# Performance work log

Measured on AMD Instinct MI355X. Metric: run time of the kernel, lower is better.

The kernel has to match this reference:

```python
import jax, jax.numpy as jnp
import numpy as np

B, T, N, F = 4096, 64, 8, 4
H = 64           # GRU hidden
EID = 16         # id embedding dim
CM = 32          # comm message dim
D = H + EID + CM # 112, attention dim
INV_SQRT_D = 1.0 / np.sqrt(112.0)


def setup_inputs() -> dict:
    key = jax.random.key(0)
    ks = jax.random.split(key, 24)
    def rn(k, shape, s=0.05):
        return jax.random.normal(k, shape, jnp.float32) * s
    return {
        "seq": jax.random.normal(ks[0], (B, T, N, F), jnp.float32),
        # GRU (torch layout: W_ih [3H,F], W_hh [3H,H], gates ordered r,z,n)
        "W_ih": rn(ks[1], (3 * H, F)), "W_hh": rn(ks[2], (3 * H, H)),
        "b_ih": rn(ks[3], (3 * H,)), "b_hh": rn(ks[4], (3 * H,)),
        "embed": rn(ks[5], (8, EID)),
        "Wm": rn(ks[6], (CM, H + EID)), "bm": rn(ks[7], (CM,)),
        "Wq": rn(ks[8], (D, D)), "bq": rn(ks[9], (D,)),
        "Wk": rn(ks[10], (D, D)), "bk": rn(ks[11], (D,)),
        "Wv": rn(ks[12], (D, D)), "bv": rn(ks[13], (D,)),
        "W1": rn(ks[14], (128, D)), "b1": rn(ks[15], (128,)),
        "W2": rn(ks[16], (128, 128)), "b2": rn(ks[17], (128,)),
        "Wmean": rn(ks[18], (2, 128)), "bmean": rn(ks[19], (2,)),
        "Wval": rn(ks[20], (1, 128)), "bval": rn(ks[21], (1,)),
    }


def _policy(seq, W_ih, W_hh, b_ih, b_hh, embed, Wm, bm,
            Wq, bq, Wk, bk, Wv, bv, W1, b1, W2, b2, Wmean, bmean, Wval, bval):
    Bb, Tt, Nn, Ff = seq.shape
    # Faithful to torch: raw view [B,T,N,F] -> [B*N,T,F] (no permute)
    x = seq.reshape(Bb * Nn, Tt, Ff)
    # Precompute all input-to-hidden projections once: [BN, T, 3H]
    x_proj = jnp.einsum('btf,gf->btg', x, W_ih) + b_ih

    def step(h, xp):
        gh = h @ W_hh.T + b_hh
        xr, xz, xn = jnp.split(xp, 3, axis=-1)
        hr, hz, hn = jnp.split(gh, 3, axis=-1)
        r = jax.nn.sigmoid(xr + hr)
        z = jax.nn.sigmoid(xz + hz)
        n = jnp.tanh(xn + r * hn)
        return (1.0 - z) * n + z * h, None

    h0 = jnp.zeros((Bb * Nn, H), seq.dtype)
    hT, _ = jax.lax.scan(step, h0, jnp.swapaxes(x_proj, 0, 1))  # carry == out[:, -1]
    h = hT.reshape(Bb, Nn, H)

    id_emb = jnp.broadcast_to(embed[:Nn], (Bb, Nn, EID))
    msgs = jnp.concatenate([h, id_emb], axis=-1) @ Wm.T + bm      # [B,N,32]
    c = jnp.broadcast_to(msgs.mean(axis=1, keepdims=True), (Bb, Nn, CM))
    h = jnp.concatenate([h, id_emb, c], axis=-1)                   # [B,N,112]

    Q = h @ Wq.T + bq
    K = h @ Wk.T + bk
    V = h @ Wv.T + bv
    attn = jax.nn.softmax(jnp.einsum('bnd,bmd->bnm', Q, K) * INV_SQRT_D, axis=-1)
    h = jnp.einsum('bnm,bmd->bnd', attn, V)

    h = jax.nn.relu(h @ W1.T + b1)
    h = jax.nn.relu(h @ W2.T + b2)
    return (h @ Wmean.T + bmean, h @ Wval.T + bval)


def reference(seq, W_ih, W_hh, b_ih, b_hh, embed, Wm, bm,
              Wq, bq, Wk, bk, Wv, bv, W1, b1, W2, b2, Wmean, bmean, Wval, bval):
    return _policy(seq, W_ih, W_hh, b_ih, b_hh, embed, Wm, bm,
                   Wq, bq, Wk, bk, Wv, bv, W1, b1, W2, b2,
                   Wmean, bmean, Wval, bval)
```

## Files before the change

### kernel.cpp

```cpp
#include <hip/hip_runtime.h>


typedef float f32x4 __attribute__((ext_vector_type(4)));
typedef short bf16x8 __attribute__((ext_vector_type(8)));

#define MFMA16 __builtin_amdgcn_mfma_f32_16x16x32_bf16
#define LOG2E 1.44269504088896f
#define INV_SQRT_D 0.09449111825230679f

__device__ __forceinline__ short f2bf(float f) {
    union { float f; unsigned u; } v; v.f = f;
    unsigned r = v.u + 0x7fffu + ((v.u >> 16) & 1u);
    return (short)(r >> 16);
}
__device__ __forceinline__ short f2bf_hu(float f) {
    union { float f; unsigned u; } v; v.f = f;
    return (short)((v.u + 0x8000u) >> 16);
}
__device__ __forceinline__ float fexp2(float x) { return __builtin_amdgcn_exp2f(x); }
__device__ __forceinline__ float frcp(float x)  { return __builtin_amdgcn_rcpf(x); }
__device__ __forceinline__ void lds_fence() {
    __asm__ __volatile__("s_waitcnt lgkmcnt(0)" ::: "memory");
}
__device__ __forceinline__ int launder(int x) {
    __asm__ __volatile__("" : "+v"(x));
    return x;
}

__global__ void conv_kernel(
    const float* __restrict__ Wm, const float* __restrict__ Wq,
    const float* __restrict__ Wk, const float* __restrict__ Wv,
    const float* __restrict__ W1, const float* __restrict__ W2,
    const float* __restrict__ Wmean, const float* __restrict__ Wval,
    unsigned short* __restrict__ wf)
{
    int gid = blockIdx.x * 256 + threadIdx.x;
    if (gid >= 158 * 64) return;
    int fid = gid >> 6, lane = gid & 63;
    int l15 = lane & 15, q = lane >> 4;

    short out[8] = {0,0,0,0,0,0,0,0};
    if (fid < 154) {
        const float* W; int nrows, Klim, idx;
        if (fid < 6)        { W = Wm; nrows = 32;  Klim = 80;  idx = fid;       }
        else if (fid < 34)  { W = Wq; nrows = 112; Klim = 112; idx = fid - 6;   }
        else if (fid < 62)  { W = Wk; nrows = 112; Klim = 112; idx = fid - 34;  }
        else if (fid < 90)  { W = Wv; nrows = 112; Klim = 112; idx = fid - 62;  }
        else if (fid < 122) { W = W1; nrows = 128; Klim = 112; idx = fid - 90;  }
        else                { W = W2; nrows = 128; Klim = 128; idx = fid - 122; }
        int nch = (fid < 6) ? 3 : 4;
        int ct = idx / nch, ch = idx - ct * nch;
        int g = ct * 16 + l15, k0 = ch * 32 + q * 8;
        if (g < nrows && (k0 + 8) <= Klim) {
            const float* wp = W + (size_t)g * Klim + k0;
            #pragma unroll
            for (int u = 0; u < 8; ++u) out[u] = f2bf(wp[u]);
        }
    } else {
        int ch = fid - 154, k0 = ch * 32 + q * 8;
        const float* wp = (l15 == 0) ? Wmean : (l15 == 1) ? (Wmean + 128)
                          : (l15 == 2) ? Wval : nullptr;
        if (wp) {
            #pragma unroll
            for (int u = 0; u < 8; ++u) out[u] = f2bf(wp[k0 + u]);
        }
    }
    *(bf16x8*)(wf + ((size_t)fid * 64 + lane) * 8) = *(bf16x8*)out;
}

__global__ __launch_bounds__(256, 2)
void policy_kernel(
    const float* __restrict__ seq,
    const float* __restrict__ W_ih, const float* __restrict__ W_hh,
    const float* __restrict__ b_ih, const float* __restrict__ b_hh,
    const float* __restrict__ embed,
    const unsigned short* __restrict__ wf,
    const float* __restrict__ bm, const float* __restrict__ bq,
    const float* __restrict__ bk, const float* __restrict__ bv,
    const float* __restrict__ b1, const float* __restrict__ b2,
    const float* __restrict__ bmean, const float* __restrict__ bval,
    float* __restrict__ out)
{
    __shared__ short R1s[4][16][136];
    __shared__ short R2s[4][16][136];
    __shared__ short R3s[4][16][136];
    __shared__ short Pbs[4][16][40];
    __shared__ short C2[12][64][8];

    const int tid  = threadIdx.x;
    const int wv   = tid >> 6;
    const int lane = tid & 63;
    const int l15  = lane & 15;
    const int q    = lane >> 4;
    const int seqbase = (blockIdx.x * 4 + wv) * 16;

    short (*R1)[136] = R1s[wv];
    short (*R2)[136] = R2s[wv];
    short (*R3)[136] = R3s[wv];
    short (*Pb)[40]  = Pbs[wv];
    const f32x4 zz = {0.f, 0.f, 0.f, 0.f};

    const float sc_rz = -LOG2E;
    const float sc_n  = 2.0f * LOG2E;

    {
        int* p;
        p = (int*)&R1[0][0]; for (int i = lane; i < 1088; i += 64) p[i] = 0;
        p = (int*)&R2[0][0]; for (int i = lane; i < 1088; i += 64) p[i] = 0;
        p = (int*)&R3[0][0]; for (int i = lane; i < 1088; i += 64) p[i] = 0;
        p = (int*)&Pb[0][0]; for (int i = lane; i < 320;  i += 64) p[i] = 0;
    }
    {
        int row = lane >> 2, j0 = (lane & 3) * 4;
        f32x4 e = *(const f32x4*)(embed + (row & 7) * 16 + j0);
        #pragma unroll
        for (int u = 0; u < 4; ++u) R1[row][64 + j0 + u] = f2bf(e[u]);
    }

    if (wv == 0) {
        #pragma unroll
        for (int j = 0; j < 8; ++j) {
            int g = j * 16 + l15;
            short f2[8] = {0,0,0,0,0,0,0,0};
            if (q == 0) {
                #pragma unroll
                for (int u = 0; u < 4; ++u) f2[u] = f2bf(W_ih[g * 4 + u] * sc_rz);
                f2[4] = f2bf((b_ih[g] + b_hh[g]) * sc_rz);
            }
            *(bf16x8*)&C2[j][lane][0] = *(bf16x8*)f2;
        }
        #pragma unroll
        for (int j2 = 0; j2 < 4; ++j2) {
            int g = 128 + j2 * 16 + l15;
            short f2[8] = {0,0,0,0,0,0,0,0};
            if (q == 0) {
                #pragma unroll
                for (int u = 0; u < 4; ++u) f2[u] = f2bf(W_ih[g * 4 + u] * sc_n);
                f2[4] = f2bf(b_ih[g] * sc_n);
            }
            *(bf16x8*)&C2[8 + j2][lane][0] = *(bf16x8*)f2;
        }
    }

    bf16x8 Bh[12][2];
    float bhh_n[4];
    #pragma unroll
    for (int j = 0; j < 12; ++j) {
        int g = j * 16 + l15;
        float s = (j < 8) ? sc_rz : sc_n;
        #pragma unroll
        for (int c = 0; c < 2; ++c) {
            const float* wp = W_hh + g * 64 + c * 32 + q * 8;
            bf16x8 f;
            #pragma unroll
            for (int u = 0; u < 8; ++u) f[u] = f2bf(wp[u] * s);
            Bh[j][c] = f;
        }
    }
    #pragma unroll
    for (int j2 = 0; j2 < 4; ++j2)
        bhh_n[j2] = b_hh[128 + j2 * 16 + l15] * sc_n;

    __syncthreads();

    const short onebf = 0x3f80;
    float h[4][4];
    #pragma unroll
    for (int j = 0; j < 4; ++j)
        #pragma unroll
        for (int r = 0; r < 4; ++r) h[j][r] = 0.f;

    const short* C2base = &C2[0][0][0];
    f32x4 xc = *(const f32x4*)(seq + (size_t)(seqbase + l15) * 256);

    for (int t = 0; t < 64; ++t) {
        int tn = (t < 63) ? t + 1 : 63;
        f32x4 xnext = *(const f32x4*)(seq + (size_t)(seqbase + l15) * 256 + tn * 4);

        bf16x8 A0 = *(const bf16x8*)&R1[l15][q * 8];
        bf16x8 A1 = *(const bf16x8*)&R1[l15][32 + q * 8];
        bf16x8 A2;
        A2[0] = f2bf_hu(xc[0]); A2[1] = f2bf_hu(xc[1]);
        A2[2] = f2bf_hu(xc[2]); A2[3] = f2bf_hu(xc[3]);
        A2[4] = onebf; A2[5] = 0; A2[6] = 0; A2[7] = 0;

        #pragma unroll
        for (int j = 0; j < 4; ++j) {
            bf16x8 c2r = *(const bf16x8*)(C2base + launder(((j    ) * 64 + lane) * 8));
            bf16x8 c2z = *(const bf16x8*)(C2base + launder(((4 + j) * 64 + lane) * 8));
            bf16x8 c2n = *(const bf16x8*)(C2base + launder(((8 + j) * 64 + lane) * 8));

            f32x4 ar = MFMA16(A2, c2r, zz, 0, 0, 0);
            ar = MFMA16(A0, Bh[j][0], ar, 0, 0, 0);
            ar = MFMA16(A1, Bh[j][1], ar, 0, 0, 0);
            f32x4 az = MFMA16(A2, c2z, zz, 0, 0, 0);
            az = MFMA16(A0, Bh[4 + j][0], az, 0, 0, 0);
            az = MFMA16(A1, Bh[4 + j][1], az, 0, 0, 0);
            f32x4 an = MFMA16(A0, Bh[8 + j][0], zz, 0, 0, 0);
            an = MFMA16(A1, Bh[8 + j][1], an, 0, 0, 0);
            f32x4 ax = MFMA16(A2, c2n, zz, 0, 0, 0);

            #pragma unroll
            for (int r = 0; r < 4; ++r) {
                float e_r  = fexp2(ar[r]);
                float rg   = frcp(1.f + e_r);
                float e_z  = fexp2(az[r]);
                float anb  = an[r] + bhh_n[j];
                float npre = fmaf(rg, anb, ax[r]);
                float e_t  = fexp2(npre);
                float tp   = e_t + 1.f;
                float tm   = e_t - 1.f;
                float hv   = h[j][r];
                float num  = fmaf(hv, tp, e_z * tm);
                float den  = fmaf(tp, e_z, tp);
                float hnew = num * frcp(den);
                h[j][r] = hnew;
                R1[q * 4 + r][16 * j + l15] = f2bf_hu(hnew);
            }
        }
        xc = xnext;
    }
    lds_fence();

    auto ld = [&](int fid) -> bf16x8 {
        return *(const bf16x8*)(wf + ((size_t)fid * 64 + lane) * 8);
    };

    #pragma unroll
    for (int ct = 0; ct < 2; ++ct) {
        f32x4 acc = zz;
        #pragma unroll
        for (int ch = 0; ch < 3; ++ch) {
            bf16x8 a = *(const bf16x8*)&R1[l15][ch * 32 + q * 8];
            acc = MFMA16(a, ld(ct * 3 + ch), acc, 0, 0, 0);
        }
        float s = acc[0] + acc[1] + acc[2] + acc[3];
        s += __shfl_xor(s, 16, 64);
        float cv = 0.125f * s + bm[16 * ct + l15];
        short cb = f2bf_hu(cv);
        #pragma unroll
        for (int r = 0; r < 4; ++r) R1[q * 4 + r][80 + 16 * ct + l15] = cb;
    }
    lds_fence();

    #pragma unroll
    for (int ct = 0; ct < 7; ++ct) {
        f32x4 aq = zz, ak = zz;
        #pragma unroll
        for (int ch = 0; ch < 4; ++ch) {
            bf16x8 a = *(const bf16x8*)&R1[l15][ch * 32 + q * 8];
            aq = MFMA16(a, ld(6  + ct * 4 + ch), aq, 0, 0, 0);
            ak = MFMA16(a, ld(34 + ct * 4 + ch), ak, 0, 0, 0);
        }
        int col = 16 * ct + l15;
        float biq = bq[col], bik = bk[col];
        #pragma unroll
        for (int r = 0; r < 4; ++r) {
            int row = q * 4 + r;
            R2[row][col] = f2bf_hu((aq[r] + biq) * INV_SQRT_D);
            R3[row][col] = f2bf_hu(ak[r] + bik);
        }
    }
    lds_fence();

    {
        f32x4 acc = zz;
        #pragma unroll
        for (int ch = 0; ch < 4; ++ch) {
            bf16x8 a = *(const bf16x8*)&R2[l15][ch * 32 + q * 8];
            bf16x8 b = *(const bf16x8*)&R3[l15][ch * 32 + q * 8];
            acc = MFMA16(a, b, acc, 0, 0, 0);
        }
        bool collow = (l15 < 8);
        #pragma unroll
        for (int r = 0; r < 4; ++r) {
            int rl = q * 4 + r;
            bool valid = ((rl < 8) == collow);
            float v = acc[r];
            float m = v;
            m = fmaxf(m, __shfl_xor(m, 1, 64));
            m = fmaxf(m, __shfl_xor(m, 2, 64));
            m = fmaxf(m, __shfl_xor(m, 4, 64));
            float e = fexp2(LOG2E * (v - m));
            float s = e;
            s += __shfl_xor(s, 1, 64);
            s += __shfl_xor(s, 2, 64);
            s += __shfl_xor(s, 4, 64);
            float pv = valid ? e * frcp(s) : 0.f;
            Pb[rl][l15] = f2bf_hu(pv);
        }
    }
    lds_fence();

    {
        short* VtR = &R2[0][0];
        #pragma unroll
        for (int ct = 0; ct < 7; ++ct) {
            f32x4 av = zz;
            #pragma unroll
            for (int ch = 0; ch < 4; ++ch) {
                bf16x8 a = *(const bf16x8*)&R1[l15][ch * 32 + q * 8];
                av = MFMA16(a, ld(62 + ct * 4 + ch), av, 0, 0, 0);
            }
            int col = 16 * ct + l15;
            float biv = bv[col];
            #pragma unroll
            for (int r = 0; r < 4; ++r)
                VtR[col * 18 + q * 4 + r] = f2bf_hu(av[r] + biv);
        }
    }
    lds_fence();

    {
        const short* VtR = &R2[0][0];
        bf16x8 a = *(const bf16x8*)&Pb[l15][q * 8];
        #pragma unroll
        for (int ct = 0; ct < 7; ++ct) {
            bf16x8 b = *(const bf16x8*)(VtR + (16 * ct + l15) * 18 + q * 8);
            f32x4 acc = MFMA16(a, b, zz, 0, 0, 0);
            #pragma unroll
            for (int r = 0; r < 4; ++r) R1[q * 4 + r][16 * ct + l15] = f2bf_hu(acc[r]);
        }
    }
    lds_fence();

    #pragma unroll
    for (int ct = 0; ct < 8; ++ct) {
        f32x4 acc = zz;
        #pragma unroll
        for (int ch = 0; ch < 4; ++ch) {
            bf16x8 a = *(const bf16x8*)&R1[l15][ch * 32 + q * 8];
            acc = MFMA16(a, ld(90 + ct * 4 + ch), acc, 0, 0, 0);
        }
        float bias = b1[16 * ct + l15];
        #pragma unroll
        for (int r = 0; r < 4; ++r)
            R2[q * 4 + r][16 * ct + l15] = f2bf_hu(fmaxf(acc[r] + bias, 0.f));
    }
    lds_fence();

    #pragma unroll
    for (int ct = 0; ct < 8; ++ct) {
        f32x4 acc = zz;
        #pragma unroll
        for (int ch = 0; ch < 4; ++ch) {
            bf16x8 a = *(const bf16x8*)&R2[l15][ch * 32 + q * 8];
            acc = MFMA16(a, ld(122 + ct * 4 + ch), acc, 0, 0, 0);
        }
        float bias = b2[16 * ct + l15];
        #pragma unroll
        for (int r = 0; r < 4; ++r)
            R3[q * 4 + r][16 * ct + l15] = f2bf_hu(fmaxf(acc[r] + bias, 0.f));
    }
    lds_fence();

    {
        f32x4 acc = zz;
        #pragma unroll
        for (int ch = 0; ch < 4; ++ch) {
            bf16x8 a = *(const bf16x8*)&R3[l15][ch * 32 + q * 8];
            acc = MFMA16(a, ld(154 + ch), acc, 0, 0, 0);
        }
        if (l15 < 3) {
            float bias = (l15 == 0) ? bmean[0] : (l15 == 1) ? bmean[1] : bval[0];
            #pragma unroll
            for (int r = 0; r < 4; ++r) {
                int A = seqbase + q * 4 + r;
                float v = acc[r] + bias;
                if (l15 < 2) out[(size_t)A * 2 + l15] = v;
                else         out[65536 + A] = v;
            }
        }
    }
}

extern "C" void kernel_launch(void* const* d_in, const int* in_sizes, int n_in,
                              void* d_out, int out_size, void* d_ws, size_t ws_size,
                              hipStream_t stream) {
    const float* seq   = (const float*)d_in[0];
    const float* W_ih  = (const float*)d_in[1];
    const float* W_hh  = (const float*)d_in[2];
    const float* b_ih  = (const float*)d_in[3];
    const float* b_hh  = (const float*)d_in[4];
    const float* embed = (const float*)d_in[5];
    const float* Wm    = (const float*)d_in[6];
    const float* bm    = (const float*)d_in[7];
    const float* Wq    = (const float*)d_in[8];
    const float* bq    = (const float*)d_in[9];
    const float* Wk    = (const float*)d_in[10];
    const float* bk    = (const float*)d_in[11];
    const float* Wv    = (const float*)d_in[12];
    const float* bv    = (const float*)d_in[13];
    const float* W1    = (const float*)d_in[14];
    const float* b1    = (const float*)d_in[15];
    const float* W2    = (const float*)d_in[16];
    const float* b2    = (const float*)d_in[17];
    const float* Wmean = (const float*)d_in[18];
    const float* bmean = (const float*)d_in[19];
    const float* Wval  = (const float*)d_in[20];
    const float* bval  = (const float*)d_in[21];

    unsigned short* wf = (unsigned short*)d_ws;

    conv_kernel<<<40, 256, 0, stream>>>(Wm, Wq, Wk, Wv, W1, W2, Wmean, Wval, wf);
    policy_kernel<<<512, 256, 0, stream>>>(seq, W_ih, W_hh, b_ih, b_hh, embed, wf,
                                           bm, bq, bk, bv, b1, b2, bmean, bval,
                                           (float*)d_out);
}
```

Measured before the change: 236.2 us.

## Split each GRU sequence tile across two waves with ping-pong hidden state buffers

Each 16-sequence GRU tile is now handled by a pair of waves, each computing half of the hidden units (two of four 16-column groups). The hidden state ping-pongs between two LDS buffers, and a workgroup barrier after every timestep keeps the pair in step. The grid doubles and launch bounds rise to four blocks per CU. This halves the serial per-wave work and register pressure, which should improve latency hiding. The cost is 64 barriers per sequence, and the second wave of each pair sits idle during the tail MLP stage.

```diff
diff --git a/kernel.cpp b/kernel.cpp
--- a/kernel.cpp
+++ b/kernel.cpp
@@ -21,6 +21,9 @@
 __device__ __forceinline__ float frcp(float x)  { return __builtin_amdgcn_rcpf(x); }
 __device__ __forceinline__ void lds_fence() {
     __asm__ __volatile__("s_waitcnt lgkmcnt(0)" ::: "memory");
+}
+__device__ __forceinline__ void step_barrier() {
+    __asm__ __volatile__("s_waitcnt lgkmcnt(0)\n\ts_barrier" ::: "memory");
 }
 __device__ __forceinline__ int launder(int x) {
     __asm__ __volatile__("" : "+v"(x));
@@ -68,7 +71,7 @@
     *(bf16x8*)(wf + ((size_t)fid * 64 + lane) * 8) = *(bf16x8*)out;
 }
 
-__global__ __launch_bounds__(256, 2)
+__global__ __launch_bounds__(256, 4)
 void policy_kernel(
     const float* __restrict__ seq,
     const float* __restrict__ W_ih, const float* __restrict__ W_hh,
@@ -81,146 +84,154 @@
     const float* __restrict__ bmean, const float* __restrict__ bval,
     float* __restrict__ out)
 {
-    __shared__ short R1s[4][16][136];
-    __shared__ short R2s[4][16][136];
-    __shared__ short R3s[4][16][136];
-    __shared__ short Pbs[4][16][40];
-    __shared__ short C2[12][64][8];
+    __shared__ short R1s[2][16][136];
+    __shared__ short Hps[2][16][72];
+    __shared__ short R2s[2][16][136];
+    __shared__ short R3s[2][16][136];
+    __shared__ short Pbs[2][16][40];
+    __shared__ short C2sm[12][16][8];
 
     const int tid  = threadIdx.x;
     const int wv   = tid >> 6;
     const int lane = tid & 63;
     const int l15  = lane & 15;
     const int q    = lane >> 4;
-    const int seqbase = (blockIdx.x * 4 + wv) * 16;
-
-    short (*R1)[136] = R1s[wv];
-    short (*R2)[136] = R2s[wv];
-    short (*R3)[136] = R3s[wv];
-    short (*Pb)[40]  = Pbs[wv];
+    const int p    = wv >> 1;
+    const int sub  = wv & 1;
+    const int sub2 = sub * 2;
+    const int seqbase = (blockIdx.x * 2 + p) * 16;
+
+    short (*R1)[136] = R1s[p];
+    short (*Hp)[72]  = Hps[p];
+    short (*R2)[136] = R2s[p];
+    short (*R3)[136] = R3s[p];
+    short (*Pb)[40]  = Pbs[p];
+    const short* C2base = &C2sm[0][0][0];
     const f32x4 zz = {0.f, 0.f, 0.f, 0.f};
 
     const float sc_rz = -LOG2E;
     const float sc_n  = 2.0f * LOG2E;
 
     {
-        int* p;
-        p = (int*)&R1[0][0]; for (int i = lane; i < 1088; i += 64) p[i] = 0;
-        p = (int*)&R2[0][0]; for (int i = lane; i < 1088; i += 64) p[i] = 0;
-        p = (int*)&R3[0][0]; for (int i = lane; i < 1088; i += 64) p[i] = 0;
-        p = (int*)&Pb[0][0]; for (int i = lane; i < 320;  i += 64) p[i] = 0;
-    }
-    {
+        int* z;
+        z = (int*)&R1[0][0]; for (int i = lane + 64 * sub; i < 1088; i += 128) z[i] = 0;
+        z = (int*)&R2[0][0]; for (int i = lane + 64 * sub; i < 1088; i += 128) z[i] = 0;
+        z = (int*)&R3[0][0]; for (int i = lane + 64 * sub; i < 1088; i += 128) z[i] = 0;
+        z = (int*)&Pb[0][0]; for (int i = lane + 64 * sub; i < 320;  i += 128) z[i] = 0;
+    }
+    if (sub == 0) {
         int row = lane >> 2, j0 = (lane & 3) * 4;
         f32x4 e = *(const f32x4*)(embed + (row & 7) * 16 + j0);
         #pragma unroll
         for (int u = 0; u < 4; ++u) R1[row][64 + j0 + u] = f2bf(e[u]);
     }
-
-    if (wv == 0) {
-        #pragma unroll
-        for (int j = 0; j < 8; ++j) {
-            int g = j * 16 + l15;
-            short f2[8] = {0,0,0,0,0,0,0,0};
-            if (q == 0) {
-                #pragma unroll
-                for (int u = 0; u < 4; ++u) f2[u] = f2bf(W_ih[g * 4 + u] * sc_rz);
-                f2[4] = f2bf((b_ih[g] + b_hh[g]) * sc_rz);
+    if (tid < 192) {
+        int j = tid >> 4, l = tid & 15, g = j * 16 + l;
+        float s = (j < 8) ? sc_rz : sc_n;
+        short f[8] = {0,0,0,0,0,0,0,0};
+        #pragma unroll
+        for (int u = 0; u < 4; ++u) f[u] = f2bf(W_ih[g * 4 + u] * s);
+        f[4] = f2bf(((j < 8) ? (b_ih[g] + b_hh[g]) : b_ih[g]) * s);
+        *(bf16x8*)&C2sm[j][l][0] = *(bf16x8*)f;
+    }
+
+    bf16x8 Bhr[2][2], Bhz[2][2], Bhn[2][2];
+    float bhh2[2];
+    #pragma unroll
+    for (int jj = 0; jj < 2; ++jj) {
+        int j = sub2 + jj;
+        #pragma unroll
+        for (int c = 0; c < 2; ++c) {
+            const float* wr = W_hh + (j * 16 + l15) * 64 + c * 32 + q * 8;
+            const float* wz = W_hh + ((4 + j) * 16 + l15) * 64 + c * 32 + q * 8;
+            const float* wn = W_hh + ((8 + j) * 16 + l15) * 64 + c * 32 + q * 8;
+            bf16x8 fr, fz, fn;
+            #pragma unroll
+            for (int u = 0; u < 8; ++u) {
+                fr[u] = f2bf(wr[u] * sc_rz);
+                fz[u] = f2bf(wz[u] * sc_rz);
+                fn[u] = f2bf(wn[u] * sc_n);
             }
-            *(bf16x8*)&C2[j][lane][0] = *(bf16x8*)f2;
-        }
-        #pragma unroll
-        for (int j2 = 0; j2 < 4; ++j2) {
-            int g = 128 + j2 * 16 + l15;
-            short f2[8] = {0,0,0,0,0,0,0,0};
-            if (q == 0) {
-                #pragma unroll
-                for (int u = 0; u < 4; ++u) f2[u] = f2bf(W_ih[g * 4 + u] * sc_n);
-                f2[4] = f2bf(b_ih[g] * sc_n);
-            }
-            *(bf16x8*)&C2[8 + j2][lane][0] = *(bf16x8*)f2;
-        }
-    }
-
-    bf16x8 Bh[12][2];
-    float bhh_n[4];
-    #pragma unroll
-    for (int j = 0; j < 12; ++j) {
-        int g = j * 16 + l15;
-        float s = (j < 8) ? sc_rz : sc_n;
-        #pragma unroll
-        for (int c = 0; c < 2; ++c) {
-            const float* wp = W_hh + g * 64 + c * 32 + q * 8;
-            bf16x8 f;
-            #pragma unroll
-            for (int u = 0; u < 8; ++u) f[u] = f2bf(wp[u] * s);
-            Bh[j][c] = f;
-        }
-    }
-    #pragma unroll
-    for (int j2 = 0; j2 < 4; ++j2)
-        bhh_n[j2] = b_hh[128 + j2 * 16 + l15] * sc_n;
+            Bhr[jj][c] = fr; Bhz[jj][c] = fz; Bhn[jj][c] = fn;
+        }
+        bhh2[jj] = b_hh[128 + j * 16 + l15] * sc_n;
+    }
 
     __syncthreads();
 
     const short onebf = 0x3f80;
-    float h[4][4];
-    #pragma unroll
-    for (int j = 0; j < 4; ++j)
-        #pragma unroll
-        for (int r = 0; r < 4; ++r) h[j][r] = 0.f;
-
-    const short* C2base = &C2[0][0][0];
-    f32x4 xc = *(const f32x4*)(seq + (size_t)(seqbase + l15) * 256);
-
-    for (int t = 0; t < 64; ++t) {
-        int tn = (t < 63) ? t + 1 : 63;
-        f32x4 xnext = *(const f32x4*)(seq + (size_t)(seqbase + l15) * 256 + tn * 4);
-
-        bf16x8 A0 = *(const bf16x8*)&R1[l15][q * 8];
-        bf16x8 A1 = *(const bf16x8*)&R1[l15][32 + q * 8];
-        bf16x8 A2;
-        A2[0] = f2bf_hu(xc[0]); A2[1] = f2bf_hu(xc[1]);
-        A2[2] = f2bf_hu(xc[2]); A2[3] = f2bf_hu(xc[3]);
-        A2[4] = onebf; A2[5] = 0; A2[6] = 0; A2[7] = 0;
-
-        #pragma unroll
-        for (int j = 0; j < 4; ++j) {
-            bf16x8 c2r = *(const bf16x8*)(C2base + launder(((j    ) * 64 + lane) * 8));
-            bf16x8 c2z = *(const bf16x8*)(C2base + launder(((4 + j) * 64 + lane) * 8));
-            bf16x8 c2n = *(const bf16x8*)(C2base + launder(((8 + j) * 64 + lane) * 8));
-
-            f32x4 ar = MFMA16(A2, c2r, zz, 0, 0, 0);
-            ar = MFMA16(A0, Bh[j][0], ar, 0, 0, 0);
-            ar = MFMA16(A1, Bh[j][1], ar, 0, 0, 0);
-            f32x4 az = MFMA16(A2, c2z, zz, 0, 0, 0);
-            az = MFMA16(A0, Bh[4 + j][0], az, 0, 0, 0);
-            az = MFMA16(A1, Bh[4 + j][1], az, 0, 0, 0);
-            f32x4 an = MFMA16(A0, Bh[8 + j][0], zz, 0, 0, 0);
-            an = MFMA16(A1, Bh[8 + j][1], an, 0, 0, 0);
-            f32x4 ax = MFMA16(A2, c2n, zz, 0, 0, 0);
-
-            #pragma unroll
-            for (int r = 0; r < 4; ++r) {
-                float e_r  = fexp2(ar[r]);
-                float rg   = frcp(1.f + e_r);
-                float e_z  = fexp2(az[r]);
-                float anb  = an[r] + bhh_n[j];
-                float npre = fmaf(rg, anb, ax[r]);
-                float e_t  = fexp2(npre);
-                float tp   = e_t + 1.f;
-                float tm   = e_t - 1.f;
-                float hv   = h[j][r];
-                float num  = fmaf(hv, tp, e_z * tm);
-                float den  = fmaf(tp, e_z, tp);
-                float hnew = num * frcp(den);
-                h[j][r] = hnew;
-                R1[q * 4 + r][16 * j + l15] = f2bf_hu(hnew);
-            }
-        }
-        xc = xnext;
-    }
-    lds_fence();
+    float h[2][4];
+    #pragma unroll
+    for (int jj = 0; jj < 2; ++jj)
+        #pragma unroll
+        for (int r = 0; r < 4; ++r) h[jj][r] = 0.f;
+
+    const float* myseq = seq + (size_t)(seqbase + l15) * 256;
+
+#define GSTEP(HC, CS, HN, NS, XV)                                              \
+    do {                                                                       \
+        bf16x8 A0 = *(const bf16x8*)((HC) + l15 * (CS) + q * 8);               \
+        bf16x8 A1 = *(const bf16x8*)((HC) + l15 * (CS) + 32 + q * 8);          \
+        bf16x8 A2;                                                             \
+        if (q == 0) {                                                          \
+            A2[0] = f2bf_hu((XV)[0]); A2[1] = f2bf_hu((XV)[1]);                \
+            A2[2] = f2bf_hu((XV)[2]); A2[3] = f2bf_hu((XV)[3]);                \
+            A2[4] = onebf; A2[5] = 0; A2[6] = 0; A2[7] = 0;                    \
+        } else {                                                               \
+            A2[0]=0;A2[1]=0;A2[2]=0;A2[3]=0;A2[4]=0;A2[5]=0;A2[6]=0;A2[7]=0;   \
+        }                                                                      \
+        _Pragma("unroll")                                                      \
+        for (int jj = 0; jj < 2; ++jj) {                                       \
+            int j = sub2 + jj;                                                 \
+            bf16x8 c2r = *(const bf16x8*)(C2base + launder(((j)      * 16 + l15) * 8)); \
+            bf16x8 c2z = *(const bf16x8*)(C2base + launder(((4 + j)  * 16 + l15) * 8)); \
+            bf16x8 c2x = *(const bf16x8*)(C2base + launder(((8 + j)  * 16 + l15) * 8)); \
+            f32x4 ar = MFMA16(A2, c2r, zz, 0, 0, 0);                           \
+            ar = MFMA16(A0, Bhr[jj][0], ar, 0, 0, 0);                          \
+            ar = MFMA16(A1, Bhr[jj][1], ar, 0, 0, 0);                          \
+            f32x4 az = MFMA16(A2, c2z, zz, 0, 0, 0);                           \
+            az = MFMA16(A0, Bhz[jj][0], az, 0, 0, 0);                          \
+            az = MFMA16(A1, Bhz[jj][1], az, 0, 0, 0);                          \
+            f32x4 an = MFMA16(A0, Bhn[jj][0], zz, 0, 0, 0);                    \
+            an = MFMA16(A1, Bhn[jj][1], an, 0, 0, 0);                          \
+            f32x4 ax = MFMA16(A2, c2x, zz, 0, 0, 0);                           \
+            _Pragma("unroll")                                                  \
+            for (int r = 0; r < 4; ++r) {                                      \
+                float e_r  = fexp2(ar[r]);                                     \
+                float rg   = frcp(1.f + e_r);                                  \
+                float e_z  = fexp2(az[r]);                                     \
+                float anb  = an[r] + bhh2[jj];                                 \
+                float npre = fmaf(rg, anb, ax[r]);                             \
+                float e_t  = fexp2(npre);                                      \
+                float tp   = e_t + 1.f;                                        \
+                float tm   = e_t - 1.f;                                        \
+                float hv   = h[jj][r];                                         \
+                float num  = fmaf(hv, tp, e_z * tm);                           \
+                float den  = fmaf(tp, e_z, tp);                                \
+                float hnew = num * frcp(den);                                  \
+                h[jj][r] = hnew;                                               \
+                (HN)[(q * 4 + r) * (NS) + 16 * j + l15] = f2bf_hu(hnew);       \
+            }                                                                  \
+            __builtin_amdgcn_sched_barrier(0);                                 \
+        }                                                                      \
+    } while (0)
+
+    f32x4 xc = *(const f32x4*)myseq;
+    #pragma unroll 1
+    for (int kk = 0; kk < 32; ++kk) {
+        int t = 2 * kk;
+        f32x4 xa = *(const f32x4*)(myseq + (t + 1) * 4);
+        GSTEP(&R1[0][0], 136, &Hp[0][0], 72, xc);
+        step_barrier();
+        int t2 = (t + 2 < 64) ? t + 2 : 63;
+        f32x4 xb = *(const f32x4*)(myseq + t2 * 4);
+        GSTEP(&Hp[0][0], 72, &R1[0][0], 136, xa);
+        step_barrier();
+        xc = xb;
+    }
+#undef GSTEP
+
+    if (sub != 0) return;
 
     auto ld = [&](int fid) -> bf16x8 {
         return *(const bf16x8*)(wf + ((size_t)fid * 64 + lane) * 8);
@@ -403,7 +414,7 @@
     unsigned short* wf = (unsigned short*)d_ws;
 
     conv_kernel<<<40, 256, 0, stream>>>(Wm, Wq, Wk, Wv, W1, W2, Wmean, Wval, wf);
-    policy_kernel<<<512, 256, 0, stream>>>(seq, W_ih, W_hh, b_ih, b_hh, embed, wf,
-                                           bm, bq, bk, bv, b1, b2, bmean, bval,
-                                           (float*)d_out);
-}
+    policy_kernel<<<1024, 256, 0, stream>>>(seq, W_ih, W_hh, b_ih, b_hh, embed, wf,
+                                            bm, bq, bk, bv, b1, b2, bmean, bval,
+                                            (float*)d_out);
+}
```

Result: slower. 247.9 us (+5.0%).

## Transpose GRU recurrence MFMA, keep hidden state in registers via bpermute

Applied to the files above, without the earlier changes.

The GRU step now uses the weights as the MFMA A operand, read from a shared LDS table, and the hidden state as the B operand. Each step rebuilds the B operand from packed bf16 registers with ds_bpermute, so the per-step LDS write and read of h is gone and the 48 W_hh fragments no longer occupy registers. The b_hh n-gate bias is folded into the input MFMA through an extra constant column, and the LDS buffers are merged into one union reused after the recurrence. The cost is eight bpermutes per step plus weight fragment LDS loads on every MFMA, which may bottleneck on LDS bandwidth or latency.

```diff
diff --git a/kernel.cpp b/kernel.cpp
--- a/kernel.cpp
+++ b/kernel.cpp
@@ -17,6 +17,10 @@
     union { float f; unsigned u; } v; v.f = f;
     return (short)((v.u + 0x8000u) >> 16);
 }
+__device__ __forceinline__ unsigned packbf(float a, float b) {
+    union { float f; unsigned u; } x, y; x.f = a; y.f = b;
+    return ((y.u + 0x8000u) & 0xffff0000u) | ((x.u + 0x8000u) >> 16);
+}
 __device__ __forceinline__ float fexp2(float x) { return __builtin_amdgcn_exp2f(x); }
 __device__ __forceinline__ float frcp(float x)  { return __builtin_amdgcn_rcpf(x); }
 __device__ __forceinline__ void lds_fence() {
@@ -26,6 +30,8 @@
     __asm__ __volatile__("" : "+v"(x));
     return x;
 }
+
+union i4h8 { int i[4]; bf16x8 h; };
 
 __global__ void conv_kernel(
     const float* __restrict__ Wm, const float* __restrict__ Wq,
@@ -81,11 +87,7 @@
     const float* __restrict__ bmean, const float* __restrict__ bval,
     float* __restrict__ out)
 {
-    __shared__ short R1s[4][16][136];
-    __shared__ short R2s[4][16][136];
-    __shared__ short R3s[4][16][136];
-    __shared__ short Pbs[4][16][40];
-    __shared__ short C2[12][64][8];
+    __shared__ __align__(16) short U[28672];
 
     const int tid  = threadIdx.x;
     const int wv   = tid >> 6;
@@ -93,133 +95,146 @@
     const int l15  = lane & 15;
     const int q    = lane >> 4;
     const int seqbase = (blockIdx.x * 4 + wv) * 16;
-
-    short (*R1)[136] = R1s[wv];
-    short (*R2)[136] = R2s[wv];
-    short (*R3)[136] = R3s[wv];
-    short (*Pb)[40]  = Pbs[wv];
     const f32x4 zz = {0.f, 0.f, 0.f, 0.f};
 
     const float sc_rz = -LOG2E;
     const float sc_n  = 2.0f * LOG2E;
 
-    {
-        int* p;
-        p = (int*)&R1[0][0]; for (int i = lane; i < 1088; i += 64) p[i] = 0;
-        p = (int*)&R2[0][0]; for (int i = lane; i < 1088; i += 64) p[i] = 0;
-        p = (int*)&R3[0][0]; for (int i = lane; i < 1088; i += 64) p[i] = 0;
-        p = (int*)&Pb[0][0]; for (int i = lane; i < 320;  i += 64) p[i] = 0;
-    }
-    {
-        int row = lane >> 2, j0 = (lane & 3) * 4;
-        f32x4 e = *(const f32x4*)(embed + (row & 7) * 16 + j0);
-        #pragma unroll
-        for (int u = 0; u < 4; ++u) R1[row][64 + j0 + u] = f2bf(e[u]);
-    }
-
-    if (wv == 0) {
-        #pragma unroll
-        for (int j = 0; j < 8; ++j) {
-            int g = j * 16 + l15;
-            short f2[8] = {0,0,0,0,0,0,0,0};
-            if (q == 0) {
+    for (int it = 0; it < 10; ++it) {
+        int row = it * 256 + tid;
+        int f = row >> 6, ln = row & 63;
+        int l = ln & 15, qq = ln >> 4;
+        short v[8] = {0,0,0,0,0,0,0,0};
+        if (f < 24) {
+            int jg = f >> 1, c = f & 1;
+            float s = (jg < 8) ? sc_rz : sc_n;
+            const float* wp = W_hh + (jg * 16 + l) * 64 + c * 32 + qq * 8;
+            #pragma unroll
+            for (int u = 0; u < 8; ++u) v[u] = f2bf(wp[u] * s);
+        } else if (f < 36) {
+            int jx = f - 24;
+            if (qq == 0) {
+                float s = (jx < 8) ? sc_rz : sc_n;
+                int g = jx * 16 + l;
                 #pragma unroll
-                for (int u = 0; u < 4; ++u) f2[u] = f2bf(W_ih[g * 4 + u] * sc_rz);
-                f2[4] = f2bf((b_ih[g] + b_hh[g]) * sc_rz);
+                for (int u = 0; u < 4; ++u) v[u] = f2bf(W_ih[g * 4 + u] * s);
+                v[4] = f2bf(((jx < 8) ? (b_ih[g] + b_hh[g]) : b_ih[g]) * s);
             }
-            *(bf16x8*)&C2[j][lane][0] = *(bf16x8*)f2;
-        }
-        #pragma unroll
-        for (int j2 = 0; j2 < 4; ++j2) {
-            int g = 128 + j2 * 16 + l15;
-            short f2[8] = {0,0,0,0,0,0,0,0};
-            if (q == 0) {
-                #pragma unroll
-                for (int u = 0; u < 4; ++u) f2[u] = f2bf(W_ih[g * 4 + u] * sc_n);
-                f2[4] = f2bf(b_ih[g] * sc_n);
-            }
-            *(bf16x8*)&C2[8 + j2][lane][0] = *(bf16x8*)f2;
-        }
-    }
-
-    bf16x8 Bh[12][2];
-    float bhh_n[4];
-    #pragma unroll
-    for (int j = 0; j < 12; ++j) {
-        int g = j * 16 + l15;
-        float s = (j < 8) ? sc_rz : sc_n;
-        #pragma unroll
-        for (int c = 0; c < 2; ++c) {
-            const float* wp = W_hh + g * 64 + c * 32 + q * 8;
-            bf16x8 f;
-            #pragma unroll
-            for (int u = 0; u < 8; ++u) f[u] = f2bf(wp[u] * s);
-            Bh[j][c] = f;
-        }
-    }
-    #pragma unroll
-    for (int j2 = 0; j2 < 4; ++j2)
-        bhh_n[j2] = b_hh[128 + j2 * 16 + l15] * sc_n;
-
+        } else {
+            int jn = f - 36;
+            if (qq == 0) v[5] = f2bf(b_hh[128 + jn * 16 + l] * sc_n);
+        }
+        *(bf16x8*)&U[row * 8] = *(bf16x8*)v;
+    }
     __syncthreads();
 
-    const short onebf = 0x3f80;
+    unsigned Ph[4][2] = {{0u,0u},{0u,0u},{0u,0u},{0u,0u}};
     float h[4][4];
     #pragma unroll
-    for (int j = 0; j < 4; ++j)
-        #pragma unroll
-        for (int r = 0; r < 4; ++r) h[j][r] = 0.f;
-
-    const short* C2base = &C2[0][0][0];
-    f32x4 xc = *(const f32x4*)(seq + (size_t)(seqbase + l15) * 256);
+    for (int jt = 0; jt < 4; ++jt)
+        #pragma unroll
+        for (int r = 0; r < 4; ++r) h[jt][r] = 0.f;
+
+    const int srcA = (((lane >> 4) & 1) * 32 + l15) * 4;
+    const int srcB = srcA + 64;
+    const bool qlow = (q < 2);
+    const float* myseq = seq + (size_t)(seqbase + l15) * 256;
+
+#define LDW(f) (*(const bf16x8*)(Wb + (f) * 512))
+#define BP(a, v) __builtin_amdgcn_ds_bpermute((a), (int)(v))
+
+    auto pull = [&](const unsigned* Plo, const unsigned* Phi) -> bf16x8 {
+        int aL0 = BP(srcA, Plo[0]), aL1 = BP(srcA, Plo[1]);
+        int bL0 = BP(srcB, Plo[0]), bL1 = BP(srcB, Plo[1]);
+        int aH0 = BP(srcA, Phi[0]), aH1 = BP(srcA, Phi[1]);
+        int bH0 = BP(srcB, Phi[0]), bH1 = BP(srcB, Phi[1]);
+        i4h8 u;
+        u.i[0] = qlow ? aL0 : aH0;
+        u.i[1] = qlow ? aL1 : aH1;
+        u.i[2] = qlow ? bL0 : bH0;
+        u.i[3] = qlow ? bL1 : bH1;
+        return u.h;
+    };
+
+    f32x4 xc = *(const f32x4*)myseq;
 
     for (int t = 0; t < 64; ++t) {
         int tn = (t < 63) ? t + 1 : 63;
-        f32x4 xnext = *(const f32x4*)(seq + (size_t)(seqbase + l15) * 256 + tn * 4);
-
-        bf16x8 A0 = *(const bf16x8*)&R1[l15][q * 8];
-        bf16x8 A1 = *(const bf16x8*)&R1[l15][32 + q * 8];
-        bf16x8 A2;
-        A2[0] = f2bf_hu(xc[0]); A2[1] = f2bf_hu(xc[1]);
-        A2[2] = f2bf_hu(xc[2]); A2[3] = f2bf_hu(xc[3]);
-        A2[4] = onebf; A2[5] = 0; A2[6] = 0; A2[7] = 0;
-
-        #pragma unroll
-        for (int j = 0; j < 4; ++j) {
-            bf16x8 c2r = *(const bf16x8*)(C2base + launder(((j    ) * 64 + lane) * 8));
-            bf16x8 c2z = *(const bf16x8*)(C2base + launder(((4 + j) * 64 + lane) * 8));
-            bf16x8 c2n = *(const bf16x8*)(C2base + launder(((8 + j) * 64 + lane) * 8));
-
-            f32x4 ar = MFMA16(A2, c2r, zz, 0, 0, 0);
-            ar = MFMA16(A0, Bh[j][0], ar, 0, 0, 0);
-            ar = MFMA16(A1, Bh[j][1], ar, 0, 0, 0);
-            f32x4 az = MFMA16(A2, c2z, zz, 0, 0, 0);
-            az = MFMA16(A0, Bh[4 + j][0], az, 0, 0, 0);
-            az = MFMA16(A1, Bh[4 + j][1], az, 0, 0, 0);
-            f32x4 an = MFMA16(A0, Bh[8 + j][0], zz, 0, 0, 0);
-            an = MFMA16(A1, Bh[8 + j][1], an, 0, 0, 0);
-            f32x4 ax = MFMA16(A2, c2n, zz, 0, 0, 0);
+        f32x4 xnext = *(const f32x4*)(myseq + tn * 4);
+
+        const short* Wb = U + launder(lane * 8);
+
+        i4h8 xb;
+        unsigned xu0 = packbf(xc[0], xc[1]);
+        unsigned xu1 = packbf(xc[2], xc[3]);
+        xb.i[0] = (q == 0) ? (int)xu0 : 0;
+        xb.i[1] = (q == 0) ? (int)xu1 : 0;
+        xb.i[2] = (q == 0) ? 0x3f803f80 : 0;
+        xb.i[3] = 0;
+        bf16x8 xB = xb.h;
+
+        bf16x8 Bh0 = pull(Ph[0], Ph[1]);
+        bf16x8 Bh1 = pull(Ph[2], Ph[3]);
+
+        #pragma unroll
+        for (int jt = 0; jt < 4; ++jt) {
+            f32x4 ar = MFMA16(LDW(24 + jt), xB, zz, 0, 0, 0);
+            ar = MFMA16(LDW(jt * 2),     Bh0, ar, 0, 0, 0);
+            ar = MFMA16(LDW(jt * 2 + 1), Bh1, ar, 0, 0, 0);
+            f32x4 az = MFMA16(LDW(28 + jt), xB, zz, 0, 0, 0);
+            az = MFMA16(LDW((4 + jt) * 2),     Bh0, az, 0, 0, 0);
+            az = MFMA16(LDW((4 + jt) * 2 + 1), Bh1, az, 0, 0, 0);
+            f32x4 an = MFMA16(LDW(36 + jt), xB, zz, 0, 0, 0);
+            an = MFMA16(LDW((8 + jt) * 2),     Bh0, an, 0, 0, 0);
+            an = MFMA16(LDW((8 + jt) * 2 + 1), Bh1, an, 0, 0, 0);
+            f32x4 ax = MFMA16(LDW(32 + jt), xB, zz, 0, 0, 0);
 
             #pragma unroll
             for (int r = 0; r < 4; ++r) {
                 float e_r  = fexp2(ar[r]);
                 float rg   = frcp(1.f + e_r);
                 float e_z  = fexp2(az[r]);
-                float anb  = an[r] + bhh_n[j];
-                float npre = fmaf(rg, anb, ax[r]);
+                float npre = fmaf(rg, an[r], ax[r]);
                 float e_t  = fexp2(npre);
                 float tp   = e_t + 1.f;
                 float tm   = e_t - 1.f;
-                float hv   = h[j][r];
+                float hv   = h[jt][r];
                 float num  = fmaf(hv, tp, e_z * tm);
                 float den  = fmaf(tp, e_z, tp);
-                float hnew = num * frcp(den);
-                h[j][r] = hnew;
-                R1[q * 4 + r][16 * j + l15] = f2bf_hu(hnew);
+                h[jt][r] = num * frcp(den);
             }
+            Ph[jt][0] = packbf(h[jt][0], h[jt][1]);
+            Ph[jt][1] = packbf(h[jt][2], h[jt][3]);
         }
         xc = xnext;
     }
+
+    bf16x8 Hc0 = pull(Ph[0], Ph[1]);
+    bf16x8 Hc1 = pull(Ph[2], Ph[3]);
+#undef LDW
+#undef BP
+
+    __syncthreads();
+
+    short (*R1)[136] = (short(*)[136])(U + wv * 7168);
+    short (*R2)[136] = (short(*)[136])(U + wv * 7168 + 2176);
+    short (*R3)[136] = (short(*)[136])(U + wv * 7168 + 4352);
+    short (*Pb)[40]  = (short(*)[40]) (U + wv * 7168 + 6528);
+
+    *(bf16x8*)&R1[l15][q * 8]      = Hc0;
+    *(bf16x8*)&R1[l15][32 + q * 8] = Hc1;
+    {
+        const float* ep = embed + (l15 & 7) * 16 + q * 4;
+        #pragma unroll
+        for (int u = 0; u < 4; ++u) R1[l15][64 + q * 4 + u] = f2bf(ep[u]);
+    }
+    const bf16x8 z8 = {0,0,0,0,0,0,0,0};
+    if (q < 2) {
+        *(bf16x8*)&R1[l15][112 + q * 8] = z8;
+        *(bf16x8*)&R2[l15][112 + q * 8] = z8;
+        *(bf16x8*)&R3[l15][112 + q * 8] = z8;
+    }
+    if (q < 3) *(bf16x8*)&Pb[l15][16 + q * 8] = z8;
     lds_fence();
 
     auto ld = [&](int fid) -> bf16x8 {
```

Result: slower. 243.8 us (+3.3%).
